# Optimization experiments

Measured on AMD Instinct MI355X. Metric: run time of the kernel, lower is better.

Reference implementation:

```python
import jax, jax.numpy as jnp
import numpy as np

B, C, K, H, W = 32, 256, 64, 56, 56


def setup_inputs() -> dict:
    key = jax.random.key(0)
    k1, k2, k3, k4 = jax.random.split(key, 4)
    main_out = jax.random.normal(k1, (B, C, H, W), dtype=jnp.float32)
    dup_out = jax.random.normal(k2, (B, K, H, W), dtype=jnp.float32)
    # buffers: per-channel valid ranges with min <= max
    min_vals = -jnp.abs(jax.random.uniform(k3, (C,), dtype=jnp.float32))
    max_vals = jnp.abs(jax.random.uniform(k4, (C,), dtype=jnp.float32)) + 0.5
    vulnerable_idx = jnp.arange(K, dtype=jnp.int32)  # first K channels are duplicated
    return {
        "main_out": main_out,
        "dup_out": dup_out,
        "min_vals": min_vals,
        "max_vals": max_vals,
        "vulnerable_idx": vulnerable_idx,
    }


def reference(main_out, dup_out, min_vals, max_vals, vulnerable_idx):
    # nan->0 (inf handled like torch.nan_to_num defaults: clamped to finite max)
    main = jnp.nan_to_num(main_out, nan=0.0)
    dup = jnp.nan_to_num(dup_out, nan=0.0)

    lo = min_vals[None, :, None, None]   # [1,C,1,1]
    hi = max_vals[None, :, None, None]

    # non-vulnerable path: zero out-of-range values (applied to all channels,
    # then vulnerable channels are overwritten below)
    out = jnp.where((main >= lo) & (main <= hi), main, jnp.zeros((), main.dtype))

    # vulnerable channels: compare main vs duplicate
    m = main[:, vulnerable_idx]          # [B,K,H,W]
    d = dup                              # [B,K,H,W]
    lov = min_vals[vulnerable_idx][None, :, None, None]
    hiv = max_vals[vulnerable_idx][None, :, None, None]
    m_valid = (m >= lov) & (m <= hiv)
    d_valid = (d >= lov) & (d <= hiv)

    # both valid and differing -> min(m,d); only d valid -> d;
    # m valid (alone or both-equal) -> m; neither -> 0
    res = jnp.where(
        m_valid & d_valid & (m != d), jnp.minimum(m, d),
        jnp.where(d_valid & ~m_valid, d,
                  jnp.where(m_valid, m, jnp.zeros((), m.dtype))))

    return out.at[:, vulnerable_idx].set(res)
```

## Files before the change

### kernel.cpp

```cpp
#include <hip/hip_runtime.h>

constexpr int BB  = 32;
constexpr int CC  = 256;
constexpr int HWN = 56 * 56;
constexpr int HW4 = HWN / 4;

__global__ void build_inv_kernel(const int* __restrict__ vidx, int K,
                                 int* __restrict__ inv) {
    int t = threadIdx.x;
    if (t < CC) inv[t] = -1;
    __syncthreads();
    if (t < K) inv[vidx[t]] = t;
}

__global__ __launch_bounds__(256) void edac_kernel(
    const float* __restrict__ mainp,
    const float* __restrict__ dupp,
    const float* __restrict__ lov,
    const float* __restrict__ hiv,
    const int*   __restrict__ inv,
    float*       __restrict__ out,
    int K)
{
    const int bc = blockIdx.x;
    const int b  = bc >> 8;
    const int c  = bc & (CC - 1);

    const float lo = lov[c];
    const float hi = hiv[c];
    const int   k  = inv[c];

    const float4* mp = (const float4*)(mainp + (size_t)bc * HWN);
    float4*       op = (float4*)(out   + (size_t)bc * HWN);

    if (k >= 0) {
        const float4* dp = (const float4*)(dupp + ((size_t)b * K + k) * HWN);
        for (int j = threadIdx.x; j < HW4; j += 256) {
            float4 m = mp[j];
            float4 d = dp[j];
            float4 r;
            #pragma unroll
            for (int e = 0; e < 4; ++e) {
                float x = ((const float*)&m)[e];
                float y = ((const float*)&d)[e];
                if (x != x) x = 0.0f;
                if (y != y) y = 0.0f;
                bool mv = (x >= lo) && (x <= hi);
                bool dv = (y >= lo) && (y <= hi);
                float res = (mv && dv && (x != y)) ? fminf(x, y)
                          : ((dv && !mv) ? y
                          : (mv ? x : 0.0f));
                ((float*)&r)[e] = res;
            }
            op[j] = r;
        }
    } else {
        for (int j = threadIdx.x; j < HW4; j += 256) {
            float4 m = mp[j];
            float4 r;
            #pragma unroll
            for (int e = 0; e < 4; ++e) {
                float x = ((const float*)&m)[e];
                if (x != x) x = 0.0f;
                bool mv = (x >= lo) && (x <= hi);
                ((float*)&r)[e] = mv ? x : 0.0f;
            }
            op[j] = r;
        }
    }
}

extern "C" void kernel_launch(void* const* d_in, const int* in_sizes, int n_in,
                              void* d_out, int out_size, void* d_ws, size_t ws_size,
                              hipStream_t stream) {
    const float* mainp = (const float*)d_in[0];
    const float* dupp  = (const float*)d_in[1];
    const float* lov   = (const float*)d_in[2];
    const float* hiv   = (const float*)d_in[3];
    const int*   vidx  = (const int*)d_in[4];
    const int    K     = in_sizes[4];

    int* inv = (int*)d_ws;

    hipLaunchKernelGGL(build_inv_kernel, dim3(1), dim3(CC), 0, stream,
                       vidx, K, inv);
    hipLaunchKernelGGL(edac_kernel, dim3(BB * CC), dim3(256), 0, stream,
                       mainp, dupp, lov, hiv, inv, (float*)d_out, K);
}
```

Baseline: 209.7 us.

## Fuse inverse-index build into main kernel, fully unroll loads, use nontemporal stores

Drops the separate single-block kernel that built the inverse channel map. Each block now finds its duplicate index with a shared-memory search over vidx. The strided loop is replaced by four explicit vector loads per thread, all issued before compute, and the outputs are written with nontemporal stores. The aims are to remove one launch plus its serialization and to increase memory-level parallelism. The search assumes K is at most 256 and adds two barriers per block.

```diff
diff --git a/kernel.cpp b/kernel.cpp
--- a/kernel.cpp
+++ b/kernel.cpp
@@ -5,12 +5,22 @@
 constexpr int HWN = 56 * 56;
 constexpr int HW4 = HWN / 4;
 
-__global__ void build_inv_kernel(const int* __restrict__ vidx, int K,
-                                 int* __restrict__ inv) {
-    int t = threadIdx.x;
-    if (t < CC) inv[t] = -1;
-    __syncthreads();
-    if (t < K) inv[vidx[t]] = t;
+typedef float v4f __attribute__((ext_vector_type(4)));
+
+__device__ __forceinline__ float edac_pair(float x, float y, float lo, float hi) {
+    if (x != x) x = 0.0f;
+    if (y != y) y = 0.0f;
+    bool mv = (x >= lo) && (x <= hi);
+    bool dv = (y >= lo) && (y <= hi);
+    return (mv && dv && (x != y)) ? fminf(x, y)
+         : ((dv && !mv) ? y
+         : (mv ? x : 0.0f));
+}
+
+__device__ __forceinline__ float edac_single(float x, float lo, float hi) {
+    if (x != x) x = 0.0f;
+    bool mv = (x >= lo) && (x <= hi);
+    return mv ? x : 0.0f;
 }
 
 __global__ __launch_bounds__(256) void edac_kernel(
@@ -18,55 +28,67 @@
     const float* __restrict__ dupp,
     const float* __restrict__ lov,
     const float* __restrict__ hiv,
-    const int*   __restrict__ inv,
+    const int*   __restrict__ vidx,
     float*       __restrict__ out,
     int K)
 {
     const int bc = blockIdx.x;
     const int b  = bc >> 8;
     const int c  = bc & (CC - 1);
+    const int t  = threadIdx.x;
+
+    __shared__ int sk;
+    if (t == 0) sk = -1;
+    __syncthreads();
+    if (t < K && vidx[t] == c) sk = t;
+    __syncthreads();
+    const int k = sk;
 
     const float lo = lov[c];
     const float hi = hiv[c];
-    const int   k  = inv[c];
 
-    const float4* mp = (const float4*)(mainp + (size_t)bc * HWN);
-    float4*       op = (float4*)(out   + (size_t)bc * HWN);
+    const v4f* mp = (const v4f*)(mainp + (size_t)bc * HWN);
+    v4f*       op = (v4f*)(out   + (size_t)bc * HWN);
+
+    const bool extra = (t < HW4 - 3 * 256);
+
+    v4f m0 = mp[t];
+    v4f m1 = mp[t + 256];
+    v4f m2 = mp[t + 512];
+    v4f m3 = extra ? mp[t + 768] : (v4f)(0.0f);
 
     if (k >= 0) {
-        const float4* dp = (const float4*)(dupp + ((size_t)b * K + k) * HWN);
-        for (int j = threadIdx.x; j < HW4; j += 256) {
-            float4 m = mp[j];
-            float4 d = dp[j];
-            float4 r;
-            #pragma unroll
-            for (int e = 0; e < 4; ++e) {
-                float x = ((const float*)&m)[e];
-                float y = ((const float*)&d)[e];
-                if (x != x) x = 0.0f;
-                if (y != y) y = 0.0f;
-                bool mv = (x >= lo) && (x <= hi);
-                bool dv = (y >= lo) && (y <= hi);
-                float res = (mv && dv && (x != y)) ? fminf(x, y)
-                          : ((dv && !mv) ? y
-                          : (mv ? x : 0.0f));
-                ((float*)&r)[e] = res;
-            }
-            op[j] = r;
+        const v4f* dp = (const v4f*)(dupp + ((size_t)b * K + k) * HWN);
+        v4f d0 = dp[t];
+        v4f d1 = dp[t + 256];
+        v4f d2 = dp[t + 512];
+        v4f d3 = extra ? dp[t + 768] : (v4f)(0.0f);
+
+        v4f r0, r1, r2, r3;
+        #pragma unroll
+        for (int e = 0; e < 4; ++e) {
+            r0[e] = edac_pair(m0[e], d0[e], lo, hi);
+            r1[e] = edac_pair(m1[e], d1[e], lo, hi);
+            r2[e] = edac_pair(m2[e], d2[e], lo, hi);
+            r3[e] = edac_pair(m3[e], d3[e], lo, hi);
         }
+        __builtin_nontemporal_store(r0, &op[t]);
+        __builtin_nontemporal_store(r1, &op[t + 256]);
+        __builtin_nontemporal_store(r2, &op[t + 512]);
+        if (extra) __builtin_nontemporal_store(r3, &op[t + 768]);
     } else {
-        for (int j = threadIdx.x; j < HW4; j += 256) {
-            float4 m = mp[j];
-            float4 r;
-            #pragma unroll
-            for (int e = 0; e < 4; ++e) {
-                float x = ((const float*)&m)[e];
-                if (x != x) x = 0.0f;
-                bool mv = (x >= lo) && (x <= hi);
-                ((float*)&r)[e] = mv ? x : 0.0f;
-            }
-            op[j] = r;
+        v4f r0, r1, r2, r3;
+        #pragma unroll
+        for (int e = 0; e < 4; ++e) {
+            r0[e] = edac_single(m0[e], lo, hi);
+            r1[e] = edac_single(m1[e], lo, hi);
+            r2[e] = edac_single(m2[e], lo, hi);
+            r3[e] = edac_single(m3[e], lo, hi);
         }
+        __builtin_nontemporal_store(r0, &op[t]);
+        __builtin_nontemporal_store(r1, &op[t + 256]);
+        __builtin_nontemporal_store(r2, &op[t + 512]);
+        if (extra) __builtin_nontemporal_store(r3, &op[t + 768]);
     }
 }
 
@@ -80,10 +102,6 @@
     const int*   vidx  = (const int*)d_in[4];
     const int    K     = in_sizes[4];
 
-    int* inv = (int*)d_ws;
-
-    hipLaunchKernelGGL(build_inv_kernel, dim3(1), dim3(CC), 0, stream,
-                       vidx, K, inv);
     hipLaunchKernelGGL(edac_kernel, dim3(BB * CC), dim3(256), 0, stream,
-                       mainp, dupp, lov, hiv, inv, (float*)d_out, K);
+                       mainp, dupp, lov, hiv, vidx, (float*)d_out, K);
 }
```

New measurement: 206.3 us. Within noise of the previous version (-1.6%).

## Flatten EDAC kernel into single grid-strided launch with nontemporal batched loads

Applied to the files above, without the earlier changes.

Replaces the per-(batch,channel) block kernel and the separate inverse-index build kernel with one flat kernel. Each thread handles 8 float4 elements spaced a full grid apart and computes channel and plane indices with a magic-number divide. Each block builds the channel ranges and inverse map in shared memory. All main loads are issued before the duplicate loads, and loads and stores use nontemporal builtins. This removes one launch and improves memory-level parallelism and occupancy, at the cost of per-element index arithmetic and divergent branches within a wave near plane boundaries.

```diff
diff --git a/kernel.cpp b/kernel.cpp
--- a/kernel.cpp
+++ b/kernel.cpp
@@ -1,71 +1,102 @@
 #include <hip/hip_runtime.h>
 
-constexpr int BB  = 32;
-constexpr int CC  = 256;
-constexpr int HWN = 56 * 56;
-constexpr int HW4 = HWN / 4;
+constexpr int BB   = 32;
+constexpr int CC   = 256;
+constexpr int HWN  = 56 * 56;
+constexpr int PL4  = HWN / 4;
+constexpr int N4   = BB * CC * PL4;
+constexpr int GRID = 3136;
+constexpr int TT   = GRID * 256;
 
-__global__ void build_inv_kernel(const int* __restrict__ vidx, int K,
-                                 int* __restrict__ inv) {
-    int t = threadIdx.x;
-    if (t < CC) inv[t] = -1;
-    __syncthreads();
-    if (t < K) inv[vidx[t]] = t;
+constexpr unsigned long long MAGIC49 = 43826197ull;
+
+typedef float v4f __attribute__((ext_vector_type(4)));
+
+__device__ __forceinline__ float edac_pair(float x, float y, float lo, float hi) {
+    if (x != x) x = 0.0f;
+    if (y != y) y = 0.0f;
+    bool mv = (x >= lo) && (x <= hi);
+    bool dv = (y >= lo) && (y <= hi);
+    return (mv && dv && (x != y)) ? fminf(x, y)
+         : ((dv && !mv) ? y
+         : (mv ? x : 0.0f));
 }
 
-__global__ __launch_bounds__(256) void edac_kernel(
+__device__ __forceinline__ float edac_single(float x, float lo, float hi) {
+    if (x != x) x = 0.0f;
+    return ((x >= lo) && (x <= hi)) ? x : 0.0f;
+}
+
+__global__ __launch_bounds__(256) void edac_flat(
     const float* __restrict__ mainp,
     const float* __restrict__ dupp,
     const float* __restrict__ lov,
     const float* __restrict__ hiv,
-    const int*   __restrict__ inv,
+    const int*   __restrict__ vidx,
     float*       __restrict__ out,
     int K)
 {
-    const int bc = blockIdx.x;
-    const int b  = bc >> 8;
-    const int c  = bc & (CC - 1);
+    __shared__ float s_lo[CC];
+    __shared__ float s_hi[CC];
+    __shared__ int   s_inv[CC];
 
-    const float lo = lov[c];
-    const float hi = hiv[c];
-    const int   k  = inv[c];
+    const int t = threadIdx.x;
+    s_lo[t]  = lov[t];
+    s_hi[t]  = hiv[t];
+    s_inv[t] = -1;
+    __syncthreads();
+    if (t < K) s_inv[vidx[t]] = t;
+    __syncthreads();
 
-    const float4* mp = (const float4*)(mainp + (size_t)bc * HWN);
-    float4*       op = (float4*)(out   + (size_t)bc * HWN);
+    const v4f* m4 = (const v4f*)mainp;
+    const v4f* d4 = (const v4f*)dupp;
+    v4f*       o4 = (v4f*)out;
 
-    if (k >= 0) {
-        const float4* dp = (const float4*)(dupp + ((size_t)b * K + k) * HWN);
-        for (int j = threadIdx.x; j < HW4; j += 256) {
-            float4 m = mp[j];
-            float4 d = dp[j];
-            float4 r;
-            #pragma unroll
-            for (int e = 0; e < 4; ++e) {
-                float x = ((const float*)&m)[e];
-                float y = ((const float*)&d)[e];
-                if (x != x) x = 0.0f;
-                if (y != y) y = 0.0f;
-                bool mv = (x >= lo) && (x <= hi);
-                bool dv = (y >= lo) && (y <= hi);
-                float res = (mv && dv && (x != y)) ? fminf(x, y)
-                          : ((dv && !mv) ? y
-                          : (mv ? x : 0.0f));
-                ((float*)&r)[e] = res;
+    const int j0 = blockIdx.x * 256 + t;
+
+    #pragma unroll
+    for (int g = 0; g < 2; ++g) {
+        int j[4];
+        v4f m[4];
+        #pragma unroll
+        for (int u = 0; u < 4; ++u) {
+            j[u] = j0 + (g * 4 + u) * TT;
+            m[u] = __builtin_nontemporal_load(&m4[j[u]]);
+        }
+
+        int   k[4];
+        float lo[4], hi[4];
+        v4f   d[4];
+        #pragma unroll
+        for (int u = 0; u < 4; ++u) {
+            const unsigned y  = ((unsigned)j[u]) >> 4;
+            const int plane   = (int)((y * MAGIC49) >> 31);
+            const int c       = plane & (CC - 1);
+            lo[u] = s_lo[c];
+            hi[u] = s_hi[c];
+            k[u]  = s_inv[c];
+            if (k[u] >= 0) {
+                const int b   = plane >> 8;
+                const int hw4 = j[u] - plane * PL4;
+                d[u] = __builtin_nontemporal_load(&d4[((size_t)b * K + k[u]) * PL4 + hw4]);
+            } else {
+                d[u] = (v4f)(0.0f);
             }
-            op[j] = r;
         }
-    } else {
-        for (int j = threadIdx.x; j < HW4; j += 256) {
-            float4 m = mp[j];
-            float4 r;
-            #pragma unroll
-            for (int e = 0; e < 4; ++e) {
-                float x = ((const float*)&m)[e];
-                if (x != x) x = 0.0f;
-                bool mv = (x >= lo) && (x <= hi);
-                ((float*)&r)[e] = mv ? x : 0.0f;
+
+        #pragma unroll
+        for (int u = 0; u < 4; ++u) {
+            v4f r;
+            if (k[u] >= 0) {
+                #pragma unroll
+                for (int e = 0; e < 4; ++e)
+                    r[e] = edac_pair(m[u][e], d[u][e], lo[u], hi[u]);
+            } else {
+                #pragma unroll
+                for (int e = 0; e < 4; ++e)
+                    r[e] = edac_single(m[u][e], lo[u], hi[u]);
             }
-            op[j] = r;
+            __builtin_nontemporal_store(r, &o4[j[u]]);
         }
     }
 }
@@ -80,10 +111,6 @@
     const int*   vidx  = (const int*)d_in[4];
     const int    K     = in_sizes[4];
 
-    int* inv = (int*)d_ws;
-
-    hipLaunchKernelGGL(build_inv_kernel, dim3(1), dim3(CC), 0, stream,
-                       vidx, K, inv);
-    hipLaunchKernelGGL(edac_kernel, dim3(BB * CC), dim3(256), 0, stream,
-                       mainp, dupp, lov, hiv, inv, (float*)d_out, K);
+    hipLaunchKernelGGL(edac_flat, dim3(GRID), dim3(256), 0, stream,
+                       mainp, dupp, lov, hiv, vidx, (float*)d_out, K);
 }
```

Measured after the change: 199.1 us. 5.1% less time.
